# Optimization experiments

Hardware: AMD Instinct MI355X
Metric: run time of the kernel (lower is better)

## Reference

```python
import jax, jax.numpy as jnp
import numpy as np
from jax import lax

EPS = 1e-5
N_WIRES, N_LAYERS = 4, 3
DIM = 2 ** N_WIRES  # 16

# Static CNOT permutations for control w, target w+1 (state @ CNOT => new[k] = old[k ^ (((k>>c)&1)<<t)])
_idx = np.arange(DIM)
CNOT_PERMS = [jnp.asarray(_idx ^ (((_idx >> w) & 1) << (w + 1))) for w in range(N_WIRES - 1)]


def conv3x3(x, w):
    # x: [B,1,H,W], w: [1,1,3,3], padding=1, no bias
    return lax.conv_general_dilated(x, w, (1, 1), 'SAME',
                                    dimension_numbers=('NCHW', 'OIHW', 'NCHW'))


def batchnorm_train(x, gamma, beta):
    # training-mode BN: batch statistics over (B,H,W), biased variance
    mean = jnp.mean(x, axis=(0, 2, 3), keepdims=True)
    var = jnp.var(x, axis=(0, 2, 3), keepdims=True)
    xn = (x - mean) * lax.rsqrt(var + EPS)
    return xn * gamma.reshape(1, -1, 1, 1) + beta.reshape(1, -1, 1, 1)


def residual_block(x, w1, g1, b1, w2, g2, b2):
    out = jax.nn.relu(batchnorm_train(conv3x3(x, w1), g1, b1))
    out = batchnorm_train(conv3x3(out, w2), g2, b2)
    return jax.nn.relu(out + x)


def quantum_feat4(theta):
    # Faithful to QuantumKernel: real state, each RZ scales by cos(theta/2)
    # (rz[0,0]==rz[1,1]==cos(theta/2)), CNOT is a bit-indexed permutation.
    # State is independent of the patch values (patch is never used).
    s = jnp.zeros(DIM, dtype=theta.dtype).at[0].set(1.0)
    for l in range(N_LAYERS):
        s = s * jnp.prod(jnp.cos(theta[l] / 2.0))  # 8 RZ scalings for this layer
        for w in range(N_WIRES - 1):
            s = s[CNOT_PERMS[w]]
    probs = s ** 2
    return probs[:4]


def setup_inputs() -> dict:
    key = jax.random.key(0)
    ks = jax.random.split(key, 12)
    B = 16384
    d = dict(
        x=jax.random.normal(ks[0], (B, 1, 28, 28), dtype=jnp.float32),
        theta=jax.random.normal(ks[1], (N_LAYERS, N_WIRES, 2), dtype=jnp.float32),
        r1_w1=jax.random.normal(ks[2], (1, 1, 3, 3), dtype=jnp.float32) * 0.3,
        r1_g1=jnp.ones((1,), jnp.float32), r1_b1=jnp.zeros((1,), jnp.float32),
        r1_w2=jax.random.normal(ks[3], (1, 1, 3, 3), dtype=jnp.float32) * 0.3,
        r1_g2=jnp.ones((1,), jnp.float32), r1_b2=jnp.zeros((1,), jnp.float32),
        r2_w1=jax.random.normal(ks[4], (1, 1, 3, 3), dtype=jnp.float32) * 0.3,
        r2_g1=jnp.ones((1,), jnp.float32), r2_b1=jnp.zeros((1,), jnp.float32),
        r2_w2=jax.random.normal(ks[5], (1, 1, 3, 3), dtype=jnp.float32) * 0.3,
        r2_g2=jnp.ones((1,), jnp.float32), r2_b2=jnp.zeros((1,), jnp.float32),
        fc_w=jax.random.normal(ks[6], (10, 784), dtype=jnp.float32) * 0.03,
        fc_b=jnp.zeros((10,), jnp.float32),
        alpha=jnp.asarray(0.5, dtype=jnp.float32),
    )
    return d


def reference(x, theta, r1_w1, r1_g1, r1_b1, r1_w2, r1_g2, r1_b2,
              r2_w1, r2_g1, r2_b1, r2_w2, r2_g2, r2_b2, fc_w, fc_b, alpha):
    B = x.shape[0]
    cls_feat = residual_block(x, r1_w1, r1_g1, r1_b1, r1_w2, r1_g2, r1_b2)
    cls_feat = residual_block(cls_feat, r2_w1, r2_g1, r2_b1, r2_w2, r2_g2, r2_b2)
    cls_flat = cls_feat.reshape(B, -1)  # [B, 784]

    # Quantum filter: kernel output ignores patch values, identical for all
    # 196 patches and all batch elements; cat along dim=1 -> tile the 4-vector.
    p4 = quantum_feat4(theta)                           # [4]
    q_feat = jnp.broadcast_to(jnp.tile(p4, 14 * 14), (B, 784))

    fused = alpha * cls_flat + (1.0 - alpha) * q_feat
    logits = fused @ fc_w.T + fc_b
    return jax.nn.log_softmax(logits, axis=-1)
```

## Files before the change

### kernel.cpp

```cpp
#include <hip/hip_runtime.h>
#include <hip/hip_fp16.h>
#include <math.h>

#define BATCH   16384
#define IMGPIX  784
#define NTOT    (BATCH * IMGPIX)
#define NSLOT   64
#define SLOTSTR 8
#define STAGE_DBL (NSLOT * SLOTSTR)
#define TROW 224
#define TGRP 6272

struct __align__(8) h4 { __half2 lo, hi; };
__device__ __forceinline__ h4 f4_to_h4(float4 v) {
    h4 r; r.lo = __floats2half2_rn(v.x, v.y); r.hi = __floats2half2_rn(v.z, v.w); return r;
}
__device__ __forceinline__ float4 h4_to_f4(h4 p) {
    float2 a = __half22float2(p.lo), b = __half22float2(p.hi);
    return make_float4(a.x, a.y, b.x, b.y);
}

__device__ __forceinline__ void wave_stats_atomic(double lsum, double lsq, double* slot) {
    #pragma unroll
    for (int off = 32; off >= 1; off >>= 1) {
        lsum += __shfl_down(lsum, off, 64);
        lsq  += __shfl_down(lsq,  off, 64);
    }
    if ((threadIdx.x & 63) == 0) {
        atomicAdd(&slot[0], lsum);
        atomicAdd(&slot[1], lsq);
    }
}

__device__ __forceinline__ float2 stats_ab(const double* __restrict__ stats_in,
                                           float gamma, float beta) {
    int lane = threadIdx.x & 63;
    double s = stats_in[lane * SLOTSTR];
    double q = stats_in[lane * SLOTSTR + 1];
    #pragma unroll
    for (int off = 32; off >= 1; off >>= 1) {
        s += __shfl_down(s, off, 64);
        q += __shfl_down(q, off, 64);
    }
    s = __shfl(s, 0, 64);
    q = __shfl(q, 0, 64);
    const double INV_N = 1.0 / (double)NTOT;
    double mean = s * INV_N;
    double var  = q * INV_N - mean * mean;
    float rstd = 1.0f / sqrtf((float)var + 1e-5f);
    float a  = gamma * rstd;
    float bb = beta - (float)mean * a;
    return make_float2(a, bb);
}

__device__ __forceinline__ float4 hrow(float wl, float wc, float wr,
                                       float L, float4 v, float R) {
    float4 h;
    h.x = fmaf(wl, L,   fmaf(wc, v.x, wr * v.y));
    h.y = fmaf(wl, v.x, fmaf(wc, v.y, wr * v.z));
    h.z = fmaf(wl, v.y, fmaf(wc, v.z, wr * v.w));
    h.w = fmaf(wl, v.z, fmaf(wc, v.w, wr * R));
    return h;
}

__device__ __forceinline__ void emit_row(__half* dst, int r, float4 o, float mf,
                                         double& lsum, double& lsq, bool act) {
    if (act) *(h4*)(dst + r * TROW) = f4_to_h4(o);
    float s4 = (o.x + o.y) + (o.z + o.w);
    float q4 = fmaf(o.x, o.x, fmaf(o.y, o.y, fmaf(o.z, o.z, o.w * o.w)));
    lsum += (double)(mf * s4);
    lsq  += (double)(mf * q4);
}

#define LANE_SETUP()                                                          \
    const int t = threadIdx.x;                                                \
    const int lane = t & 63;                                                  \
    const int widx = t >> 6;                                                  \
    const int c4   = lane & 7;                                                \
    const bool act = (c4 < 7);                                                \
    const float mf = act ? 1.f : 0.f;                                         \
    const int c4c  = c4 < 7 ? c4 : 6;          \
    const int g    = blockIdx.x & 511;                 \
    const int s    = blockIdx.x >> 9;                         \
    const int r0   = s * 7;                                                   \
    const int rtop = (r0 > 0)  ? (r0 - 1) : 0;         \
    const int rbot = (r0 < 21) ? (r0 + 7) : 27;                               \
    const int i8   = lane >> 3;                                               \
    const int G    = g * 4 + widx;                 \
    const int img  = G * 8 + i8;                                              \
    const size_t xbase = (size_t)img * IMGPIX + c4c * 4;           \
    const size_t tbR   = (size_t)G * TGRP + c4c * 32 + i8 * 4;     \
    const size_t tbW   = (size_t)G * TGRP + c4  * 32 + i8 * 4;

#define CONV_STEP(k, v)                                                       \
    {                                                                         \
        float L = __shfl_up((v).w, 1, 64);  if (c4 == 0) L = 0.f;             \
        float R = __shfl_down((v).x, 1, 64); if (c4 == 6) R = 0.f;            \
        float4 h2 = hrow(w9[6], w9[7], w9[8], L, (v), R);                     \
        float4 h1 = hrow(w9[3], w9[4], w9[5], L, (v), R);                     \
        float4 h0 = hrow(w9[0], w9[1], w9[2], L, (v), R);                     \
        accA.x += h2.x; accA.y += h2.y; accA.z += h2.z; accA.w += h2.w;       \
        if ((k) >= 2) emit_row(dst, r0 + (k) - 2, accA, mf, lsum, lsq, act);  \
        accA.x = accB.x + h1.x; accA.y = accB.y + h1.y;                       \
        accA.z = accB.z + h1.z; accA.w = accB.w + h1.w;                       \
        accB = h0;                                                            \
    }

#define HALO_ZERO(k, v)                                                       \
    if ((k) == 0 && r0 == 0)  (v) = ZERO4;                                    \
    if ((k) == 8 && r0 == 21) (v) = ZERO4;

#define ZERO4 make_float4(0.f, 0.f, 0.f, 0.f)

__global__ __launch_bounds__(256, 8) void k_conv_plain(const float* __restrict__ in,
        const float* __restrict__ w, __half* __restrict__ out,
        __half* __restrict__ x16_out, double* __restrict__ stats_out)
{
    LANE_SETUP();
    float w9[9];
    #pragma unroll
    for (int i = 0; i < 9; i++) w9[i] = w[i];
    const float* src = in + xbase;
    __half* dst  = out + tbW;
    __half* dstx = x16_out + tbW;

    float4 vb[9];
    vb[0] = *(const float4*)(src + rtop * 28);
    #pragma unroll
    for (int k = 1; k < 8; k++) vb[k] = *(const float4*)(src + (r0 - 1 + k) * 28);
    vb[8] = *(const float4*)(src + rbot * 28);
    __builtin_amdgcn_sched_barrier(0);

    float4 accA = ZERO4, accB = ZERO4;
    double lsum = 0.0, lsq = 0.0;
    #pragma unroll
    for (int k = 0; k < 9; k++) {
        float4 v = vb[k];
        if (act && k >= 1 && k <= 7)
            *(h4*)(dstx + (r0 - 1 + k) * TROW) = f4_to_h4(vb[k]);
        HALO_ZERO(k, v);
        CONV_STEP(k, v);
    }
    wave_stats_atomic(lsum, lsq, &stats_out[((blockIdx.x * 4 + widx) & (NSLOT - 1)) * SLOTSTR]);
}

__global__ __launch_bounds__(256, 8) void k_conv_affine(const __half* __restrict__ in,
        const double* __restrict__ stats_in,
        const float* __restrict__ gamma, const float* __restrict__ beta,
        const float* __restrict__ w, __half* __restrict__ out, double* __restrict__ stats_out)
{
    LANE_SETUP();
    float2 ab = stats_ab(stats_in, gamma[0], beta[0]);
    float w9[9];
    #pragma unroll
    for (int i = 0; i < 9; i++) w9[i] = w[i];
    const __half* src = in + tbR;
    __half* dst = out + tbW;

    h4 vb[9];
    vb[0] = *(const h4*)(src + rtop * TROW);
    #pragma unroll
    for (int k = 1; k < 8; k++) vb[k] = *(const h4*)(src + (r0 - 1 + k) * TROW);
    vb[8] = *(const h4*)(src + rbot * TROW);
    __builtin_amdgcn_sched_barrier(0);

    float4 accA = ZERO4, accB = ZERO4;
    double lsum = 0.0, lsq = 0.0;
    #pragma unroll
    for (int k = 0; k < 9; k++) {
        float4 r4 = h4_to_f4(vb[k]);
        float4 v;
        v.x = fmaxf(fmaf(ab.x, r4.x, ab.y), 0.f);
        v.y = fmaxf(fmaf(ab.x, r4.y, ab.y), 0.f);
        v.z = fmaxf(fmaf(ab.x, r4.z, ab.y), 0.f);
        v.w = fmaxf(fmaf(ab.x, r4.w, ab.y), 0.f);
        HALO_ZERO(k, v);
        CONV_STEP(k, v);
    }
    wave_stats_atomic(lsum, lsq, &stats_out[((blockIdx.x * 4 + widx) & (NSLOT - 1)) * SLOTSTR]);
}

__global__ __launch_bounds__(256, 8) void k_conv_resid(const __half* __restrict__ y2,
        const __half* __restrict__ x16, const double* __restrict__ stats_in,
        const float* __restrict__ gamma, const float* __restrict__ beta,
        const float* __restrict__ w, __half* __restrict__ y3_out,
        __half* __restrict__ o1_out, double* __restrict__ stats_out)
{
    LANE_SETUP();
    float2 ab = stats_ab(stats_in, gamma[0], beta[0]);
    float w9[9];
    #pragma unroll
    for (int i = 0; i < 9; i++) w9[i] = w[i];
    const __half* srcy = y2 + tbR;
    const __half* srcx = x16 + tbR;
    __half* dst  = y3_out + tbW;
    __half* dsto = o1_out + tbW;

    h4 yb[9], xb[9];
    yb[0] = *(const h4*)(srcy + rtop * TROW);
    xb[0] = *(const h4*)(srcx + rtop * TROW);
    #pragma unroll
    for (int k = 1; k < 8; k++) {
        yb[k] = *(const h4*)(srcy + (r0 - 1 + k) * TROW);
        xb[k] = *(const h4*)(srcx + (r0 - 1 + k) * TROW);
    }
    yb[8] = *(const h4*)(srcy + rbot * TROW);
    xb[8] = *(const h4*)(srcx + rbot * TROW);
    __builtin_amdgcn_sched_barrier(0);

    float4 accA = ZERO4, accB = ZERO4;
    double lsum = 0.0, lsq = 0.0;
    #pragma unroll
    for (int k = 0; k < 9; k++) {
        float4 r4 = h4_to_f4(yb[k]);
        float4 x4 = h4_to_f4(xb[k]);
        float4 v;
        v.x = fmaxf(fmaf(ab.x, r4.x, ab.y) + x4.x, 0.f);
        v.y = fmaxf(fmaf(ab.x, r4.y, ab.y) + x4.y, 0.f);
        v.z = fmaxf(fmaf(ab.x, r4.z, ab.y) + x4.z, 0.f);
        v.w = fmaxf(fmaf(ab.x, r4.w, ab.y) + x4.w, 0.f);
        HALO_ZERO(k, v);
        if (act && k >= 1 && k <= 7)
            *(h4*)(dsto + (r0 - 1 + k) * TROW) = f4_to_h4(v);
        CONV_STEP(k, v);
    }
    wave_stats_atomic(lsum, lsq, &stats_out[((blockIdx.x * 4 + widx) & (NSLOT - 1)) * SLOTSTR]);
}

__global__ __launch_bounds__(256) void k_head(const __half* __restrict__ y4,
        const __half* __restrict__ o1, const double* __restrict__ stats_in,
        const float* __restrict__ gamma, const float* __restrict__ beta,
        const float* __restrict__ fc_w, const float* __restrict__ qk,
        const float* __restrict__ alpha_p, float* __restrict__ out)
{
    __shared__ float fcK[7840];
    const int t = threadIdx.x;
    float2 ab = stats_ab(stats_in, gamma[0], beta[0]);
    for (int idx = t; idx < 7840; idx += 256) fcK[idx] = fc_w[idx];
    float alpha = alpha_p[0];
    float qkr[10];
    #pragma unroll
    for (int k = 0; k < 10; k++) qkr[k] = qk[k];
    __syncthreads();

    const int lane = t & 63;
    const int widx = t >> 6;
    const int c4   = lane & 7;
    const int i8   = lane >> 3;
    const int c4c  = c4 < 7 ? c4 : 6;
    const float mf = (c4 < 7) ? 1.f : 0.f;
    const int G    = blockIdx.x * 4 + widx;
    const size_t tb = (size_t)G * TGRP + c4c * 32 + i8 * 4;
    const __half* ya = y4 + tb;
    const __half* oa = o1 + tb;

    float acc[10];
    #pragma unroll
    for (int k = 0; k < 10; k++) acc[k] = 0.f;

    #pragma unroll 7
    for (int r = 0; r < 28; r++) {
        float4 yf = h4_to_f4(*(const h4*)(ya + r * TROW));
        float4 of = h4_to_f4(*(const h4*)(oa + r * TROW));
        float4 v;
        v.x = fmaxf(fmaf(ab.x, yf.x, ab.y) + of.x, 0.f);
        v.y = fmaxf(fmaf(ab.x, yf.y, ab.y) + of.y, 0.f);
        v.z = fmaxf(fmaf(ab.x, yf.z, ab.y) + of.z, 0.f);
        v.w = fmaxf(fmaf(ab.x, yf.w, ab.y) + of.w, 0.f);
        const float* fb = &fcK[r * 28 + c4c * 4];
        #pragma unroll
        for (int k = 0; k < 10; k++) {
            const float4 f = *(const float4*)(fb + k * 784);
            acc[k] = fmaf(v.x, f.x, fmaf(v.y, f.y, fmaf(v.z, f.z, fmaf(v.w, f.w, acc[k]))));
        }
    }
    #pragma unroll
    for (int k = 0; k < 10; k++) {
        acc[k] *= mf;
        acc[k] += __shfl_xor(acc[k], 1, 64);
        acc[k] += __shfl_xor(acc[k], 2, 64);
        acc[k] += __shfl_xor(acc[k], 4, 64);
    }
    float l[10];
    float m = -1e30f;
    #pragma unroll
    for (int k = 0; k < 10; k++) {
        l[k] = fmaf(alpha, acc[k], qkr[k]);
        m = fmaxf(m, l[k]);
    }
    float se = 0.f;
    #pragma unroll
    for (int k = 0; k < 10; k++) se += __expf(l[k] - m);
    float lse = m + __logf(se);
    if (c4 == 0) {
        int img = G * 8 + i8;
        #pragma unroll
        for (int k = 0; k < 10; k++) out[(size_t)img * 10 + k] = l[k] - lse;
    }
}

__global__ __launch_bounds__(256) void k_init(const float* __restrict__ theta,
        const float* __restrict__ fc_w, const float* __restrict__ fc_b,
        const float* __restrict__ alpha_p, float* __restrict__ qk, double* __restrict__ stats)
{
    const int t = threadIdx.x;
    for (int i = t; i < 4 * STAGE_DBL; i += 256) stats[i] = 0.0;
    __shared__ float csum[10];
    if (t < 80) {
        int k = t >> 3, oct = t & 7;
        float s = 0.f;
        #pragma unroll
        for (int i = 0; i < 25; i++) {
            int p = oct + 8 * i;
            if (p < 196) s += fc_w[k * 784 + p * 4];
        }
        s += __shfl_xor(s, 1, 64);
        s += __shfl_xor(s, 2, 64);
        s += __shfl_xor(s, 4, 64);
        if (oct == 0) csum[k] = s;
    }
    __syncthreads();
    if (t < 10) {
        float c = 1.f;
        #pragma unroll
        for (int i = 0; i < 24; i++) c *= cosf(theta[i] * 0.5f);
        float c2 = c * c;
        qk[t] = (1.f - alpha_p[0]) * c2 * csum[t] + fc_b[t];
    }
}

extern "C" void kernel_launch(void* const* d_in, const int* in_sizes, int n_in,
                              void* d_out, int out_size, void* d_ws, size_t ws_size,
                              hipStream_t stream) {
    const float* x     = (const float*)d_in[0];
    const float* theta = (const float*)d_in[1];
    const float* r1_w1 = (const float*)d_in[2];
    const float* r1_g1 = (const float*)d_in[3];
    const float* r1_b1 = (const float*)d_in[4];
    const float* r1_w2 = (const float*)d_in[5];
    const float* r1_g2 = (const float*)d_in[6];
    const float* r1_b2 = (const float*)d_in[7];
    const float* r2_w1 = (const float*)d_in[8];
    const float* r2_g1 = (const float*)d_in[9];
    const float* r2_b1 = (const float*)d_in[10];
    const float* r2_w2 = (const float*)d_in[11];
    const float* r2_g2 = (const float*)d_in[12];
    const float* r2_b2 = (const float*)d_in[13];
    const float* fc_w  = (const float*)d_in[14];
    const float* fc_b  = (const float*)d_in[15];
    const float* alpha = (const float*)d_in[16];
    float* out = (float*)d_out;

    double* stats = (double*)d_ws;
    float*  qk    = (float*)((char*)d_ws + 16384);
    __half* bufA  = (__half*)((char*)d_ws + 32768);
    __half* bufB  = bufA + (size_t)NTOT;
    __half* bufD  = bufB + (size_t)NTOT;
    __half* bufX  = bufD + (size_t)NTOT;

    double* s_y1 = stats + 0 * STAGE_DBL;
    double* s_y2 = stats + 1 * STAGE_DBL;
    double* s_y3 = stats + 2 * STAGE_DBL;
    double* s_y4 = stats + 3 * STAGE_DBL;

    k_init<<<1, 256, 0, stream>>>(theta, fc_w, fc_b, alpha, qk, stats);
    k_conv_plain<<<2048, 256, 0, stream>>>(x, r1_w1, bufA, bufX, s_y1);
    k_conv_affine<<<2048, 256, 0, stream>>>(bufA, s_y1, r1_g1, r1_b1, r1_w2, bufB, s_y2);
    k_conv_resid<<<2048, 256, 0, stream>>>(bufB, bufX, s_y2, r1_g2, r1_b2, r2_w1, bufA, bufD, s_y3);
    k_conv_affine<<<2048, 256, 0, stream>>>(bufA, s_y3, r2_g1, r2_b1, r2_w2, bufB, s_y4);
    k_head<<<512, 256, 0, stream>>>(bufB, bufD, s_y4, r2_g2, r2_b2, fc_w, qk, alpha, out);
}
```

Measured before the change: 107.2 us.

## Fuse all stages into one persistent kernel with grid-wide barriers

```diff
diff --git a/kernel.cpp b/kernel.cpp
--- a/kernel.cpp
+++ b/kernel.cpp
@@ -8,6 +8,7 @@
 #define NSLOT   64
 #define SLOTSTR 8
 #define STAGE_DBL (NSLOT * SLOTSTR)
+#define NBLK    256
 #define TROW 224
 #define TGRP 6272
 
@@ -18,6 +19,25 @@
 __device__ __forceinline__ float4 h4_to_f4(h4 p) {
     float2 a = __half22float2(p.lo), b = __half22float2(p.hi);
     return make_float4(a.x, a.y, b.x, b.y);
+}
+#define ZERO4 make_float4(0.f, 0.f, 0.f, 0.f)
+
+__device__ __forceinline__ void grid_barrier(int* bar, int* gen) {
+    __syncthreads();
+    if (threadIdx.x == 0) {
+        __threadfence();
+        int g = __hip_atomic_load(gen, __ATOMIC_ACQUIRE, __HIP_MEMORY_SCOPE_AGENT);
+        int a = __hip_atomic_fetch_add(bar, 1, __ATOMIC_ACQ_REL, __HIP_MEMORY_SCOPE_AGENT);
+        if (a == NBLK - 1) {
+            __hip_atomic_store(bar, 0, __ATOMIC_RELAXED, __HIP_MEMORY_SCOPE_AGENT);
+            __hip_atomic_fetch_add(gen, 1, __ATOMIC_ACQ_REL, __HIP_MEMORY_SCOPE_AGENT);
+        } else {
+            while (__hip_atomic_load(gen, __ATOMIC_ACQUIRE, __HIP_MEMORY_SCOPE_AGENT) == g)
+                __builtin_amdgcn_s_sleep(2);
+        }
+        __threadfence();
+    }
+    __syncthreads();
 }
 
 __device__ __forceinline__ void wave_stats_atomic(double lsum, double lsq, double* slot) {
@@ -72,100 +92,70 @@
     lsq  += (double)(mf * q4);
 }
 
-#define LANE_SETUP()                                                          \
-    const int t = threadIdx.x;                                                \
-    const int lane = t & 63;                                                  \
-    const int widx = t >> 6;                                                  \
-    const int c4   = lane & 7;                                                \
-    const bool act = (c4 < 7);                                                \
-    const float mf = act ? 1.f : 0.f;                                         \
-    const int c4c  = c4 < 7 ? c4 : 6;          \
-    const int g    = blockIdx.x & 511;                 \
-    const int s    = blockIdx.x >> 9;                         \
+__device__ __forceinline__ void conv_step(float4 v, int k, int r0, int c4,
+        const float* w9, float4& accA, float4& accB, __half* dst, float mf,
+        double& lsum, double& lsq, bool act) {
+    float L = __shfl_up(v.w, 1, 64);   if (c4 == 0) L = 0.f;
+    float R = __shfl_down(v.x, 1, 64); if (c4 == 6) R = 0.f;
+    float4 h2 = hrow(w9[6], w9[7], w9[8], L, v, R);
+    float4 h1 = hrow(w9[3], w9[4], w9[5], L, v, R);
+    float4 h0 = hrow(w9[0], w9[1], w9[2], L, v, R);
+    accA.x += h2.x; accA.y += h2.y; accA.z += h2.z; accA.w += h2.w;
+    if (k >= 2) emit_row(dst, r0 + k - 2, accA, mf, lsum, lsq, act);
+    accA.x = accB.x + h1.x; accA.y = accB.y + h1.y;
+    accA.z = accB.z + h1.z; accA.w = accB.w + h1.w;
+    accB = h0;
+}
+
+#define TASK_GEOM()                                                           \
     const int r0   = s * 7;                                                   \
-    const int rtop = (r0 > 0)  ? (r0 - 1) : 0;         \
+    const int rtop = (r0 > 0)  ? (r0 - 1) : 0;                                \
     const int rbot = (r0 < 21) ? (r0 + 7) : 27;                               \
-    const int i8   = lane >> 3;                                               \
-    const int G    = g * 4 + widx;                 \
-    const int img  = G * 8 + i8;                                              \
-    const size_t xbase = (size_t)img * IMGPIX + c4c * 4;           \
-    const size_t tbR   = (size_t)G * TGRP + c4c * 32 + i8 * 4;     \
-    const size_t tbW   = (size_t)G * TGRP + c4  * 32 + i8 * 4;
-
-#define CONV_STEP(k, v)                                                       \
-    {                                                                         \
-        float L = __shfl_up((v).w, 1, 64);  if (c4 == 0) L = 0.f;             \
-        float R = __shfl_down((v).x, 1, 64); if (c4 == 6) R = 0.f;            \
-        float4 h2 = hrow(w9[6], w9[7], w9[8], L, (v), R);                     \
-        float4 h1 = hrow(w9[3], w9[4], w9[5], L, (v), R);                     \
-        float4 h0 = hrow(w9[0], w9[1], w9[2], L, (v), R);                     \
-        accA.x += h2.x; accA.y += h2.y; accA.z += h2.z; accA.w += h2.w;       \
-        if ((k) >= 2) emit_row(dst, r0 + (k) - 2, accA, mf, lsum, lsq, act);  \
-        accA.x = accB.x + h1.x; accA.y = accB.y + h1.y;                       \
-        accA.z = accB.z + h1.z; accA.w = accB.w + h1.w;                       \
-        accB = h0;                                                            \
-    }
+    const size_t tbR = (size_t)G * TGRP + c4c * 32 + i8 * 4;                  \
+    const size_t tbW = (size_t)G * TGRP + c4  * 32 + i8 * 4;
 
 #define HALO_ZERO(k, v)                                                       \
     if ((k) == 0 && r0 == 0)  (v) = ZERO4;                                    \
     if ((k) == 8 && r0 == 21) (v) = ZERO4;
 
-#define ZERO4 make_float4(0.f, 0.f, 0.f, 0.f)
-
-__global__ __launch_bounds__(256, 8) void k_conv_plain(const float* __restrict__ in,
-        const float* __restrict__ w, __half* __restrict__ out,
-        __half* __restrict__ x16_out, double* __restrict__ stats_out)
-{
-    LANE_SETUP();
-    float w9[9];
-    #pragma unroll
-    for (int i = 0; i < 9; i++) w9[i] = w[i];
-    const float* src = in + xbase;
-    __half* dst  = out + tbW;
-    __half* dstx = x16_out + tbW;
-
+__device__ __forceinline__ void task_plain(int G, int s, int c4, int c4c, int i8,
+        bool act, float mf, const float* w9, const float* x,
+        __half* y1, __half* x16, double& lsum, double& lsq) {
+    TASK_GEOM();
+    const int img = G * 8 + i8;
+    const float* src = x + (size_t)img * IMGPIX + c4c * 4;
+    __half* dst  = y1  + tbW;
+    __half* dstx = x16 + tbW;
     float4 vb[9];
     vb[0] = *(const float4*)(src + rtop * 28);
     #pragma unroll
     for (int k = 1; k < 8; k++) vb[k] = *(const float4*)(src + (r0 - 1 + k) * 28);
     vb[8] = *(const float4*)(src + rbot * 28);
     __builtin_amdgcn_sched_barrier(0);
-
     float4 accA = ZERO4, accB = ZERO4;
-    double lsum = 0.0, lsq = 0.0;
     #pragma unroll
     for (int k = 0; k < 9; k++) {
         float4 v = vb[k];
         if (act && k >= 1 && k <= 7)
             *(h4*)(dstx + (r0 - 1 + k) * TROW) = f4_to_h4(vb[k]);
         HALO_ZERO(k, v);
-        CONV_STEP(k, v);
-    }
-    wave_stats_atomic(lsum, lsq, &stats_out[((blockIdx.x * 4 + widx) & (NSLOT - 1)) * SLOTSTR]);
-}
-
-__global__ __launch_bounds__(256, 8) void k_conv_affine(const __half* __restrict__ in,
-        const double* __restrict__ stats_in,
-        const float* __restrict__ gamma, const float* __restrict__ beta,
-        const float* __restrict__ w, __half* __restrict__ out, double* __restrict__ stats_out)
-{
-    LANE_SETUP();
-    float2 ab = stats_ab(stats_in, gamma[0], beta[0]);
-    float w9[9];
-    #pragma unroll
-    for (int i = 0; i < 9; i++) w9[i] = w[i];
+        conv_step(v, k, r0, c4, w9, accA, accB, dst, mf, lsum, lsq, act);
+    }
+}
+
+__device__ __forceinline__ void task_affine(int G, int s, int c4, int c4c, int i8,
+        bool act, float mf, const float* w9, float2 ab,
+        const __half* in, __half* out, double& lsum, double& lsq) {
+    TASK_GEOM();
     const __half* src = in + tbR;
     __half* dst = out + tbW;
-
     h4 vb[9];
     vb[0] = *(const h4*)(src + rtop * TROW);
     #pragma unroll
     for (int k = 1; k < 8; k++) vb[k] = *(const h4*)(src + (r0 - 1 + k) * TROW);
     vb[8] = *(const h4*)(src + rbot * TROW);
     __builtin_amdgcn_sched_barrier(0);
-
     float4 accA = ZERO4, accB = ZERO4;
-    double lsum = 0.0, lsq = 0.0;
     #pragma unroll
     for (int k = 0; k < 9; k++) {
         float4 r4 = h4_to_f4(vb[k]);
@@ -175,27 +165,19 @@
         v.z = fmaxf(fmaf(ab.x, r4.z, ab.y), 0.f);
         v.w = fmaxf(fmaf(ab.x, r4.w, ab.y), 0.f);
         HALO_ZERO(k, v);
-        CONV_STEP(k, v);
-    }
-    wave_stats_atomic(lsum, lsq, &stats_out[((blockIdx.x * 4 + widx) & (NSLOT - 1)) * SLOTSTR]);
-}
-
-__global__ __launch_bounds__(256, 8) void k_conv_resid(const __half* __restrict__ y2,
-        const __half* __restrict__ x16, const double* __restrict__ stats_in,
-        const float* __restrict__ gamma, const float* __restrict__ beta,
-        const float* __restrict__ w, __half* __restrict__ y3_out,
-        __half* __restrict__ o1_out, double* __restrict__ stats_out)
-{
-    LANE_SETUP();
-    float2 ab = stats_ab(stats_in, gamma[0], beta[0]);
-    float w9[9];
-    #pragma unroll
-    for (int i = 0; i < 9; i++) w9[i] = w[i];
+        conv_step(v, k, r0, c4, w9, accA, accB, dst, mf, lsum, lsq, act);
+    }
+}
+
+__device__ __forceinline__ void task_resid(int G, int s, int c4, int c4c, int i8,
+        bool act, float mf, const float* w9, float2 ab,
+        const __half* y2, const __half* x16, __half* y3, __half* o1,
+        double& lsum, double& lsq) {
+    TASK_GEOM();
     const __half* srcy = y2 + tbR;
     const __half* srcx = x16 + tbR;
-    __half* dst  = y3_out + tbW;
-    __half* dsto = o1_out + tbW;
-
+    __half* dst  = y3 + tbW;
+    __half* dsto = o1 + tbW;
     h4 yb[9], xb[9];
     yb[0] = *(const h4*)(srcy + rtop * TROW);
     xb[0] = *(const h4*)(srcx + rtop * TROW);
@@ -207,9 +189,7 @@
     yb[8] = *(const h4*)(srcy + rbot * TROW);
     xb[8] = *(const h4*)(srcx + rbot * TROW);
     __builtin_amdgcn_sched_barrier(0);
-
     float4 accA = ZERO4, accB = ZERO4;
-    double lsum = 0.0, lsq = 0.0;
     #pragma unroll
     for (int k = 0; k < 9; k++) {
         float4 r4 = h4_to_f4(yb[k]);
@@ -222,110 +202,183 @@
         HALO_ZERO(k, v);
         if (act && k >= 1 && k <= 7)
             *(h4*)(dsto + (r0 - 1 + k) * TROW) = f4_to_h4(v);
-        CONV_STEP(k, v);
-    }
-    wave_stats_atomic(lsum, lsq, &stats_out[((blockIdx.x * 4 + widx) & (NSLOT - 1)) * SLOTSTR]);
-}
-
-__global__ __launch_bounds__(256) void k_head(const __half* __restrict__ y4,
-        const __half* __restrict__ o1, const double* __restrict__ stats_in,
-        const float* __restrict__ gamma, const float* __restrict__ beta,
-        const float* __restrict__ fc_w, const float* __restrict__ qk,
-        const float* __restrict__ alpha_p, float* __restrict__ out)
+        conv_step(v, k, r0, c4, w9, accA, accB, dst, mf, lsum, lsq, act);
+    }
+}
+
+__global__ __launch_bounds__(1024, 4) void k_fused(
+        const float* __restrict__ x, const float* __restrict__ theta,
+        const float* __restrict__ w1, const float* __restrict__ g1, const float* __restrict__ b1,
+        const float* __restrict__ w2, const float* __restrict__ g2, const float* __restrict__ b2,
+        const float* __restrict__ w3, const float* __restrict__ g3, const float* __restrict__ b3,
+        const float* __restrict__ w4, const float* __restrict__ g4, const float* __restrict__ b4,
+        const float* __restrict__ fc_w, const float* __restrict__ fc_b,
+        const float* __restrict__ alpha_p,
+        __half* __restrict__ y1, __half* __restrict__ y2, __half* __restrict__ y3,
+        __half* __restrict__ y4, __half* __restrict__ o1, __half* __restrict__ x16,
+        double* __restrict__ stats, int* __restrict__ bar, int* __restrict__ gen,
+        float* __restrict__ out)
 {
-    __shared__ float fcK[7840];
-    const int t = threadIdx.x;
-    float2 ab = stats_ab(stats_in, gamma[0], beta[0]);
-    for (int idx = t; idx < 7840; idx += 256) fcK[idx] = fc_w[idx];
-    float alpha = alpha_p[0];
-    float qkr[10];
-    #pragma unroll
-    for (int k = 0; k < 10; k++) qkr[k] = qk[k];
-    __syncthreads();
-
+    __shared__ float qk_s[10];
+    __shared__ float accs[16][8][10];
+
+    const int t    = threadIdx.x;
     const int lane = t & 63;
     const int widx = t >> 6;
     const int c4   = lane & 7;
     const int i8   = lane >> 3;
+    const bool act = (c4 < 7);
+    const float mf = act ? 1.f : 0.f;
     const int c4c  = c4 < 7 ? c4 : 6;
-    const float mf = (c4 < 7) ? 1.f : 0.f;
-    const int G    = blockIdx.x * 4 + widx;
-    const size_t tb = (size_t)G * TGRP + c4c * 32 + i8 * 4;
-    const __half* ya = y4 + tb;
-    const __half* oa = o1 + tb;
-
-    float acc[10];
-    #pragma unroll
-    for (int k = 0; k < 10; k++) acc[k] = 0.f;
-
-    #pragma unroll 7
-    for (int r = 0; r < 28; r++) {
-        float4 yf = h4_to_f4(*(const h4*)(ya + r * TROW));
-        float4 of = h4_to_f4(*(const h4*)(oa + r * TROW));
-        float4 v;
-        v.x = fmaxf(fmaf(ab.x, yf.x, ab.y) + of.x, 0.f);
-        v.y = fmaxf(fmaf(ab.x, yf.y, ab.y) + of.y, 0.f);
-        v.z = fmaxf(fmaf(ab.x, yf.z, ab.y) + of.z, 0.f);
-        v.w = fmaxf(fmaf(ab.x, yf.w, ab.y) + of.w, 0.f);
-        const float* fb = &fcK[r * 28 + c4c * 4];
-        #pragma unroll
-        for (int k = 0; k < 10; k++) {
-            const float4 f = *(const float4*)(fb + k * 784);
-            acc[k] = fmaf(v.x, f.x, fmaf(v.y, f.y, fmaf(v.z, f.z, fmaf(v.w, f.w, acc[k]))));
-        }
-    }
-    #pragma unroll
-    for (int k = 0; k < 10; k++) {
-        acc[k] *= mf;
-        acc[k] += __shfl_xor(acc[k], 1, 64);
-        acc[k] += __shfl_xor(acc[k], 2, 64);
-        acc[k] += __shfl_xor(acc[k], 4, 64);
-    }
-    float l[10];
-    float m = -1e30f;
-    #pragma unroll
-    for (int k = 0; k < 10; k++) {
-        l[k] = fmaf(alpha, acc[k], qkr[k]);
-        m = fmaxf(m, l[k]);
-    }
-    float se = 0.f;
-    #pragma unroll
-    for (int k = 0; k < 10; k++) se += __expf(l[k] - m);
-    float lse = m + __logf(se);
-    if (c4 == 0) {
-        int img = G * 8 + i8;
-        #pragma unroll
-        for (int k = 0; k < 10; k++) out[(size_t)img * 10 + k] = l[k] - lse;
-    }
-}
-
-__global__ __launch_bounds__(256) void k_init(const float* __restrict__ theta,
-        const float* __restrict__ fc_w, const float* __restrict__ fc_b,
-        const float* __restrict__ alpha_p, float* __restrict__ qk, double* __restrict__ stats)
-{
-    const int t = threadIdx.x;
-    for (int i = t; i < 4 * STAGE_DBL; i += 256) stats[i] = 0.0;
-    __shared__ float csum[10];
+    const int bid  = blockIdx.x;
+
+    double* s_y1 = stats + 0 * STAGE_DBL;
+    double* s_y2 = stats + 1 * STAGE_DBL;
+    double* s_y3 = stats + 2 * STAGE_DBL;
+    double* s_y4 = stats + 3 * STAGE_DBL;
+    const int slotidx = ((bid * 16 + widx) & (NSLOT - 1)) * SLOTSTR;
+
     if (t < 80) {
         int k = t >> 3, oct = t & 7;
-        float s = 0.f;
+        float sm = 0.f;
         #pragma unroll
         for (int i = 0; i < 25; i++) {
             int p = oct + 8 * i;
-            if (p < 196) s += fc_w[k * 784 + p * 4];
-        }
-        s += __shfl_xor(s, 1, 64);
-        s += __shfl_xor(s, 2, 64);
-        s += __shfl_xor(s, 4, 64);
-        if (oct == 0) csum[k] = s;
+            if (p < 196) sm += fc_w[k * 784 + p * 4];
+        }
+        sm += __shfl_xor(sm, 1, 64);
+        sm += __shfl_xor(sm, 2, 64);
+        sm += __shfl_xor(sm, 4, 64);
+        if (oct == 0) qk_s[k] = sm;
     }
     __syncthreads();
     if (t < 10) {
         float c = 1.f;
         #pragma unroll
         for (int i = 0; i < 24; i++) c *= cosf(theta[i] * 0.5f);
-        float c2 = c * c;
-        qk[t] = (1.f - alpha_p[0]) * c2 * csum[t] + fc_b[t];
+        qk_s[t] = (1.f - alpha_p[0]) * (c * c) * qk_s[t] + fc_b[t];
+    }
+
+    {
+        float w9[9];
+        #pragma unroll
+        for (int i = 0; i < 9; i++) w9[i] = w1[i];
+        double lsum = 0.0, lsq = 0.0;
+        #pragma unroll
+        for (int tt = 0; tt < 2; tt++) {
+            int task = bid * 16 + widx + tt * 4096;
+            task_plain(task & 2047, task >> 11, c4, c4c, i8, act, mf, w9, x, y1, x16, lsum, lsq);
+        }
+        wave_stats_atomic(lsum, lsq, s_y1 + slotidx);
+    }
+    grid_barrier(bar, gen);
+
+    {
+        float2 ab = stats_ab(s_y1, g1[0], b1[0]);
+        float w9[9];
+        #pragma unroll
+        for (int i = 0; i < 9; i++) w9[i] = w2[i];
+        double lsum = 0.0, lsq = 0.0;
+        #pragma unroll
+        for (int tt = 0; tt < 2; tt++) {
+            int task = bid * 16 + widx + tt * 4096;
+            task_affine(task & 2047, task >> 11, c4, c4c, i8, act, mf, w9, ab, y1, y2, lsum, lsq);
+        }
+        wave_stats_atomic(lsum, lsq, s_y2 + slotidx);
+    }
+    grid_barrier(bar, gen);
+
+    {
+        float2 ab = stats_ab(s_y2, g2[0], b2[0]);
+        float w9[9];
+        #pragma unroll
+        for (int i = 0; i < 9; i++) w9[i] = w3[i];
+        double lsum = 0.0, lsq = 0.0;
+        #pragma unroll
+        for (int tt = 0; tt < 2; tt++) {
+            int task = bid * 16 + widx + tt * 4096;
+            task_resid(task & 2047, task >> 11, c4, c4c, i8, act, mf, w9, ab, y2, x16, y3, o1, lsum, lsq);
+        }
+        wave_stats_atomic(lsum, lsq, s_y3 + slotidx);
+    }
+    grid_barrier(bar, gen);
+
+    {
+        float2 ab = stats_ab(s_y3, g3[0], b3[0]);
+        float w9[9];
+        #pragma unroll
+        for (int i = 0; i < 9; i++) w9[i] = w4[i];
+        double lsum = 0.0, lsq = 0.0;
+        #pragma unroll
+        for (int tt = 0; tt < 2; tt++) {
+            int task = bid * 16 + widx + tt * 4096;
+            task_affine(task & 2047, task >> 11, c4, c4c, i8, act, mf, w9, ab, y3, y4, lsum, lsq);
+        }
+        wave_stats_atomic(lsum, lsq, s_y4 + slotidx);
+    }
+    grid_barrier(bar, gen);
+
+    {
+        float2 ab = stats_ab(s_y4, g4[0], b4[0]);
+        float al = alpha_p[0];
+        const int q = widx & 3;
+        #pragma unroll
+        for (int tt = 0; tt < 2; tt++) {
+            const int G = bid * 4 + (widx >> 2) + tt * 1024;
+            const size_t tb = (size_t)G * TGRP + c4c * 32 + i8 * 4;
+            float acc[10];
+            #pragma unroll
+            for (int k = 0; k < 10; k++) acc[k] = 0.f;
+            #pragma unroll
+            for (int rr = 0; rr < 7; rr++) {
+                const int r = q * 7 + rr;
+                float4 yf = h4_to_f4(*(const h4*)(y4 + tb + r * TROW));
+                float4 of = h4_to_f4(*(const h4*)(o1 + tb + r * TROW));
+                float4 v;
+                v.x = fmaxf(fmaf(ab.x, yf.x, ab.y) + of.x, 0.f);
+                v.y = fmaxf(fmaf(ab.x, yf.y, ab.y) + of.y, 0.f);
+                v.z = fmaxf(fmaf(ab.x, yf.z, ab.y) + of.z, 0.f);
+                v.w = fmaxf(fmaf(ab.x, yf.w, ab.y) + of.w, 0.f);
+                const float* fb = fc_w + r * 28 + c4c * 4;
+                #pragma unroll
+                for (int k = 0; k < 10; k++) {
+                    const float4 f = *(const float4*)(fb + k * 784);
+                    acc[k] = fmaf(v.x, f.x, fmaf(v.y, f.y, fmaf(v.z, f.z, fmaf(v.w, f.w, acc[k]))));
+                }
+            }
+            #pragma unroll
+            for (int k = 0; k < 10; k++) {
+                acc[k] *= mf;
+                acc[k] += __shfl_xor(acc[k], 1, 64);
+                acc[k] += __shfl_xor(acc[k], 2, 64);
+                acc[k] += __shfl_xor(acc[k], 4, 64);
+            }
+            if (c4 == 0) {
+                #pragma unroll
+                for (int k = 0; k < 10; k++) accs[widx][i8][k] = acc[k];
+            }
+            __syncthreads();
+            if (t < 32) {
+                int Gi = t >> 3, ii = t & 7;
+                float l[10];
+                float m = -1e30f;
+                #pragma unroll
+                for (int k = 0; k < 10; k++) {
+                    float ssum = accs[Gi * 4 + 0][ii][k] + accs[Gi * 4 + 1][ii][k]
+                               + accs[Gi * 4 + 2][ii][k] + accs[Gi * 4 + 3][ii][k];
+                    l[k] = fmaf(al, ssum, qk_s[k]);
+                    m = fmaxf(m, l[k]);
+                }
+                float se = 0.f;
+                #pragma unroll
+                for (int k = 0; k < 10; k++) se += __expf(l[k] - m);
+                float lse = m + __logf(se);
+                int img = (bid * 4 + Gi + tt * 1024) * 8 + ii;
+                #pragma unroll
+                for (int k = 0; k < 10; k++) out[(size_t)img * 10 + k] = l[k] - lse;
+            }
+            __syncthreads();
+        }
     }
 }
 
@@ -352,21 +405,25 @@
     float* out = (float*)d_out;
 
     double* stats = (double*)d_ws;
-    float*  qk    = (float*)((char*)d_ws + 16384);
-    __half* bufA  = (__half*)((char*)d_ws + 32768);
-    __half* bufB  = bufA + (size_t)NTOT;
-    __half* bufD  = bufB + (size_t)NTOT;
-    __half* bufX  = bufD + (size_t)NTOT;
-
-    double* s_y1 = stats + 0 * STAGE_DBL;
-    double* s_y2 = stats + 1 * STAGE_DBL;
-    double* s_y3 = stats + 2 * STAGE_DBL;
-    double* s_y4 = stats + 3 * STAGE_DBL;
-
-    k_init<<<1, 256, 0, stream>>>(theta, fc_w, fc_b, alpha, qk, stats);
-    k_conv_plain<<<2048, 256, 0, stream>>>(x, r1_w1, bufA, bufX, s_y1);
-    k_conv_affine<<<2048, 256, 0, stream>>>(bufA, s_y1, r1_g1, r1_b1, r1_w2, bufB, s_y2);
-    k_conv_resid<<<2048, 256, 0, stream>>>(bufB, bufX, s_y2, r1_g2, r1_b2, r2_w1, bufA, bufD, s_y3);
-    k_conv_affine<<<2048, 256, 0, stream>>>(bufA, s_y3, r2_g1, r2_b1, r2_w2, bufB, s_y4);
-    k_head<<<512, 256, 0, stream>>>(bufB, bufD, s_y4, r2_g2, r2_b2, fc_w, qk, alpha, out);
-}
+    int*    bar   = (int*)((char*)d_ws + 16384);
+    int*    gen   = bar + 1;
+    __half* base  = (__half*)((char*)d_ws + 32768);
+    __half* y1  = base;
+    __half* y2  = y1 + (size_t)NTOT;
+    __half* y3  = y2 + (size_t)NTOT;
+    __half* y4  = y3 + (size_t)NTOT;
+    __half* o1  = y4 + (size_t)NTOT;
+    __half* x16 = o1 + (size_t)NTOT;
+
+    hipMemsetAsync(d_ws, 0, 32768, stream);
+
+    k_fused<<<NBLK, 1024, 0, stream>>>(
+        x, theta,
+        r1_w1, r1_g1, r1_b1,
+        r1_w2, r1_g2, r1_b2,
+        r2_w1, r2_g1, r2_b1,
+        r2_w2, r2_g2, r2_b2,
+        fc_w, fc_b, alpha,
+        y1, y2, y3, y4, o1, x16,
+        stats, bar, gen, out);
+}
```

Result: slower. 321.4 us (+199.7%).
